# Optimization experiments

Hardware: AMD Instinct MI355X
Metric: run time of the kernel (lower is better)

The kernel has to match this reference:

```python
import jax, jax.numpy as jnp
from jax import lax
import numpy as np

BLOCK = 256
EPS = 1e-6


def rms_norm(x, w):
    var = jnp.mean(jnp.square(x), axis=-1, keepdims=True)
    return x * lax.rsqrt(var + EPS) * w


def lightning_attn(q, k, v, slope):
    # q,k,v: [b,h,n,d]; slope: [h] positive decay rates
    b, h, n, d = q.shape
    nb = n // BLOCK
    ar = jnp.arange(1, BLOCK + 1, dtype=q.dtype)          # [BLOCK]
    s = slope[:, None, None]                               # [h,1,1]
    q_decay = jnp.exp(-s * ar[:, None])                    # [h,BLOCK,1]
    k_decay = jnp.exp(-s * (BLOCK - ar)[:, None])          # [h,BLOCK,1]
    idx = ar[:, None] - ar[None, :]                        # [BLOCK,BLOCK]
    diag_decay = jnp.exp(jnp.where(idx >= 0, -s * idx, -jnp.inf))  # [h,B,B]
    block_decay = jnp.exp(-slope * BLOCK)[None, :, None, None]     # [1,h,1,1]

    def to_blocks(x):
        return jnp.moveaxis(x.reshape(b, h, nb, BLOCK, d), 2, 0)   # [nb,b,h,B,d]

    qb, kb, vb = to_blocks(q), to_blocks(k), to_blocks(v)

    def step(kv, blk):
        qi, ki, vi = blk                                   # [b,h,B,d]
        inter = jnp.einsum('bhmd,bhde->bhme', qi * q_decay, kv)
        qk = jnp.einsum('bhmd,bhkd->bhmk', qi, ki) * diag_decay
        intra = jnp.einsum('bhmk,bhke->bhme', qk, vi)
        kv_new = block_decay * kv + jnp.einsum('bhmd,bhme->bhde', ki * k_decay, vi)
        return kv_new, inter + intra

    kv0 = jnp.zeros((b, h, d, d), q.dtype)
    kv, out = lax.scan(step, kv0, (qb, kb, vb))            # out: [nb,b,h,B,d]
    out = jnp.moveaxis(out, 0, 2).reshape(b, h, n, d)
    return out, kv


def setup_inputs() -> dict:
    key = jax.random.key(0)
    ks = jax.random.split(key, 6)
    b, n, hidden, h, dh = 2, 4096, 2048, 16, 128
    return {
        'hidden_states': jax.random.normal(ks[0], (b, n, hidden), jnp.float32),
        'slope_rate': jax.random.uniform(ks[1], (h,), jnp.float32, 1e-3, 0.2),
        'w_qkv': jax.random.normal(ks[2], (3 * h * dh, hidden), jnp.float32) * 0.02,
        'w_gate': jax.random.normal(ks[3], (h * dh, hidden), jnp.float32) * 0.02,
        'w_out': jax.random.normal(ks[4], (hidden, h * dh), jnp.float32) * 0.02,
        'norm_w': jnp.ones((h * dh,), jnp.float32),
    }


def reference(hidden_states, slope_rate, w_qkv, w_gate, w_out, norm_w):
    b, n, hidden = hidden_states.shape
    h = slope_rate.shape[0]
    dh = hidden // h
    qkv = jax.nn.silu(hidden_states @ w_qkv.T)             # [b,n,3*h*dh]
    qkv = qkv.reshape(b, n, 3, h, dh)
    q = jnp.transpose(qkv[:, :, 0], (0, 2, 1, 3))          # [b,h,n,dh]
    k = jnp.transpose(qkv[:, :, 1], (0, 2, 1, 3))
    v = jnp.transpose(qkv[:, :, 2], (0, 2, 1, 3))
    attn_out, _kv = lightning_attn(q, k, v, slope_rate)
    attn_out = jnp.transpose(attn_out, (0, 2, 1, 3)).reshape(b, n, h * dh)
    out = rms_norm(attn_out, norm_w)
    gate = jax.nn.sigmoid(hidden_states @ w_gate.T)
    out = (gate * out) @ w_out.T
    return out
```

## Files before the change

### kernel.cpp

```cpp
#include <hip/hip_runtime.h>


typedef unsigned short u16;
typedef __bf16 bf16x8 __attribute__((ext_vector_type(8)));
typedef float f32x4 __attribute__((ext_vector_type(4)));

#define SEQ 4096
#define HID 2048

__device__ __forceinline__ u16 f2bf(float f) {
    union { float f; unsigned u; } v; v.f = f;
    unsigned r = v.u + 0x7fffu + ((v.u >> 16) & 1u);
    return (u16)(r >> 16);
}
__device__ __forceinline__ float bf2f(u16 u) {
    union { unsigned u; float f; } v; v.u = ((unsigned)u) << 16; return v.f;
}

typedef __attribute__((address_space(1))) unsigned char gas_u8;
typedef __attribute__((address_space(3))) unsigned char las_u8;
__device__ __forceinline__ void gld16(const void* g, void* l) {
    __builtin_amdgcn_global_load_lds((gas_u8*)g, (las_u8*)l, 16, 0, 0);
}

__global__ __launch_bounds__(256) void castk(const float* __restrict__ in,
                                             u16* __restrict__ out) {
    const size_t i = (size_t)blockIdx.x * 256 + threadIdx.x;
    const float4 f = *(const float4*)&in[i * 4];
    uint2 o;
    o.x = (unsigned)f2bf(f.x) | ((unsigned)f2bf(f.y) << 16);
    o.y = (unsigned)f2bf(f.z) | ((unsigned)f2bf(f.w) << 16);
    *(uint2*)&out[i * 4] = o;
}

template <int MODE>
__global__ __launch_bounds__(512, 2) void gemm256(const u16* __restrict__ A,
                                                  const u16* __restrict__ Bm,
                                                  void* __restrict__ Cv,
                                                  void* __restrict__ aux,
                                                  void* __restrict__ aux2) {
    constexpr int NTN = (MODE == 0) ? 32 : 8;
    constexpr int NWG = (MODE == 0) ? 1024 : 256;
    constexpr int NT  = 32;
    extern __shared__ u16 smem[];

    const int bid  = blockIdx.x;
    const int wgid = (bid & 7) * (NWG >> 3) + (bid >> 3);
    const int tm = wgid / NTN, tn = wgid % NTN;

    const int tid  = threadIdx.x;
    const int lane = tid & 63, wv = tid >> 6;
    const int quad = lane >> 4, cl = lane & 15;
    const int wm = (wv & 1) * 128, wn = (wv >> 1) * 64;

    const int srw  = tid >> 3;
    const int colo = ((tid & 7) ^ (srw & 7)) * 8;
    const u16* gA0 = A  + (size_t)(tm * 256 + srw) * HID + colo;
    const u16* gB0 = Bm + (size_t)(tn * 256 + srw) * HID + colo;

    const int x0 = ((quad       ^ (cl & 7)) * 8);
    const int x1 = (((4 + quad) ^ (cl & 7)) * 8);

    f32x4 acc[8][4];
    const f32x4 zero = {0.f, 0.f, 0.f, 0.f};
    #pragma unroll
    for (int a = 0; a < 8; a++)
        #pragma unroll
        for (int b = 0; b < 4; b++) acc[a][b] = zero;

    bf16x8 af[8], b0[4], b1[4];

    auto STG = [&](int kt, int mat, int hh) {
        const u16* g = (mat ? gB0 : gA0) + (size_t)(hh * 128) * HID + kt * 64;
        u16* l = smem + (kt & 1) * 32768 + mat * 16384 + hh * 8192 + wv * 512;
        gld16(g, l);
        gld16(g + (size_t)64 * HID, l + 4096);
    };
    auto LDA = [&](int qm, int ab) {
        #pragma unroll
        for (int mi = 0; mi < 4; mi++) {
            const int rr = (wm + qm * 64 + mi * 16 + cl) * 64 + ab;
            af[mi * 2 + 0] = *(const bf16x8*)&smem[rr + x0];
            af[mi * 2 + 1] = *(const bf16x8*)&smem[rr + x1];
        }
    };
    auto LDB = [&](bf16x8* d, int qn, int bb2) {
        #pragma unroll
        for (int ni = 0; ni < 2; ni++) {
            const int rr = (wn + qn * 32 + ni * 16 + cl) * 64 + bb2;
            d[ni * 2 + 0] = *(const bf16x8*)&smem[rr + x0];
            d[ni * 2 + 1] = *(const bf16x8*)&smem[rr + x1];
        }
    };
    auto MM = [&](int qm, int qn, const bf16x8* bv) {
        #pragma unroll
        for (int mi = 0; mi < 4; mi++)
            #pragma unroll
            for (int ni = 0; ni < 2; ni++) {
                f32x4 c = acc[qm * 4 + mi][qn * 2 + ni];
                c = __builtin_amdgcn_mfma_f32_16x16x32_bf16(af[mi * 2 + 0], bv[ni * 2 + 0], c, 0, 0, 0);
                c = __builtin_amdgcn_mfma_f32_16x16x32_bf16(af[mi * 2 + 1], bv[ni * 2 + 1], c, 0, 0, 0);
                acc[qm * 4 + mi][qn * 2 + ni] = c;
            }
    };

    STG(0, 1, 0); STG(0, 1, 1); STG(0, 0, 0); STG(0, 0, 1);
    STG(1, 1, 0); STG(1, 1, 1); STG(1, 0, 0);
    asm volatile("s_waitcnt vmcnt(6)" ::: "memory");
    __builtin_amdgcn_s_barrier();

    #pragma unroll 2
    for (int t = 0; t < NT; ++t) {
        const int ab  = (t & 1) * 32768;
        const int bb2 = ab + 16384;
        LDA(0, ab); LDB(b0, 0, bb2);
        if (t + 1 < NT) STG(t + 1, 0, 1);
        __builtin_amdgcn_s_barrier();
        asm volatile("s_waitcnt lgkmcnt(0)" ::: "memory");
        __builtin_amdgcn_s_setprio(1); MM(0, 0, b0); __builtin_amdgcn_s_setprio(0);
        __builtin_amdgcn_s_barrier();
        LDB(b1, 1, bb2);
        if (t + 2 < NT) STG(t + 2, 1, 0);
        __builtin_amdgcn_s_barrier();
        asm volatile("s_waitcnt lgkmcnt(0)" ::: "memory");
        __builtin_amdgcn_s_setprio(1); MM(0, 1, b1); __builtin_amdgcn_s_setprio(0);
        __builtin_amdgcn_s_barrier();
        LDA(1, ab);
        if (t + 2 < NT) STG(t + 2, 1, 1);
        __builtin_amdgcn_s_barrier();
        asm volatile("s_waitcnt lgkmcnt(0)" ::: "memory");
        __builtin_amdgcn_s_setprio(1); MM(1, 1, b1); __builtin_amdgcn_s_setprio(0);
        __builtin_amdgcn_s_barrier();
        if (t + 2 < NT) {
            STG(t + 2, 0, 0);
            asm volatile("s_waitcnt vmcnt(6)" ::: "memory");
        } else {
            asm volatile("s_waitcnt vmcnt(0)" ::: "memory");
        }
        __builtin_amdgcn_s_barrier();
        __builtin_amdgcn_s_setprio(1); MM(1, 0, b0); __builtin_amdgcn_s_setprio(0);
        __builtin_amdgcn_s_barrier();
    }

    if constexpr (MODE == 0) {
        const int grp = tn * 2 + (wn >> 7);
        const int which = grp >> 4, hd = grp & 15;
        const int n64 = wn & 64;
        if (which == 2) {
            const size_t bz = (size_t)((tm >> 4) * 256 + hd * 16 + (tm & 15));
            u16* tdst = (u16*)aux + bz * 32768;
            #pragma unroll
            for (int a = 0; a < 8; a++) {
                const int mm = wm + (a >> 2) * 64 + (a & 3) * 16 + quad * 4;
                #pragma unroll
                for (int b = 0; b < 4; b++) {
                    const int d = n64 + (b >> 1) * 32 + (b & 1) * 16 + cl;
                    u16 p[4];
                    #pragma unroll
                    for (int r = 0; r < 4; r++) {
                        const float x = acc[a][b][r];
                        p[r] = f2bf(x / (1.f + __expf(-x)));
                    }
                    uint2 pk;
                    pk.x = (unsigned)p[0] | ((unsigned)p[1] << 16);
                    pk.y = (unsigned)p[2] | ((unsigned)p[3] << 16);
                    *(uint2*)&tdst[(size_t)d * 256 + mm] = pk;
                }
            }
            return;
        }
        u16* dst = (which == 0) ? (u16*)Cv
                 : (which == 1) ? (u16*)Cv + (size_t)16777216
                                : (u16*)aux2;
        #pragma unroll
        for (int a = 0; a < 8; a++)
            #pragma unroll
            for (int b = 0; b < 4; b++)
                #pragma unroll
                for (int r = 0; r < 4; r++) {
                    const int m = tm * 256 + wm + (a >> 2) * 64 + (a & 3) * 16 + quad * 4 + r;
                    const int col = hd * 128 + n64 + (b >> 1) * 32 + (b & 1) * 16 + cl;
                    const float x = acc[a][b][r];
                    const float v = (which == 3) ? 1.f / (1.f + __expf(-x))
                                                 : x / (1.f + __expf(-x));
                    dst[(size_t)m * HID + col] = f2bf(v);
                }
        return;
    } else {
        float* C = (float*)Cv;
        #pragma unroll
        for (int a = 0; a < 8; a++)
            #pragma unroll
            for (int b = 0; b < 4; b++)
                #pragma unroll
                for (int r = 0; r < 4; r++) {
                    const int m = tm * 256 + wm + (a >> 2) * 64 + (a & 3) * 16 + quad * 4 + r;
                    const int n = tn * 256 + wn + (b >> 1) * 32 + (b & 1) * 16 + cl;
                    C[(size_t)m * HID + n] = acc[a][b][r];
                }
    }
}

#define M_QKV   0
#define M_P     2
#define M_INTRA 3
#define M_KVT   4
#define M_OUT   6

template <int MODE>
__global__ __launch_bounds__(256) void gemm_nt(const u16* __restrict__ A,
                                               const u16* __restrict__ Bm,
                                               void* __restrict__ Cv,
                                               const float* __restrict__ slope,
                                               int bz0,
                                               void* __restrict__ aux,
                                               void* __restrict__ aux2) {
    constexpr int NPH = (MODE == M_INTRA) ? 2 : 1;
    const int tid = threadIdx.x;
    const int tm = blockIdx.x, tn = blockIdx.y;
    const int bzl = blockIdx.z;
    const int bz  = bzl + bz0;

    int bb = 0, hh = 0, jb = 0;
    if constexpr (MODE == M_P || MODE == M_INTRA || MODE == M_KVT) {
        bb = bz >> 8; hh = (bz >> 4) & 15; jb = bz & 15;
    }

    if constexpr (MODE == M_P) {
        if (tn > tm) {
            u16* C = (u16*)Cv + (size_t)bzl * 65536 + tm * 128 * 256 + tn * 128;
            uint4 z = make_uint4(0u, 0u, 0u, 0u);
            #pragma unroll
            for (int i = 0; i < 8; i++) {
                int f = tid + 256 * i;
                int row = f >> 4, c8 = (f & 15) * 8;
                *(uint4*)&C[row * 256 + c8] = z;
            }
            return;
        }
    }

    __shared__ u16 smem[8192];
    u16 (*As)[32] = (u16(*)[32])smem;
    u16 (*Bs)[32] = (u16(*)[32])(smem + 4096);

    const int lane = tid & 63, wv = tid >> 6;
    const int wm = (wv & 1) * 64, wn = (wv >> 1) * 64;
    const int quad = lane >> 4, cl = lane & 15;
    const int lr = lane >> 2;
    const int lc = (lane & 3) * 8;
    u16* lA = &As[wv * 32][0];
    u16* lB = &Bs[wv * 32][0];

    f32x4 acc[4][4];
    const f32x4 zero = {0.f, 0.f, 0.f, 0.f};
    #pragma unroll
    for (int mi = 0; mi < 4; mi++)
        #pragma unroll
        for (int ni = 0; ni < 4; ni++) acc[mi][ni] = zero;

    #pragma unroll
    for (int ph = 0; ph < NPH; ph++) {
        const u16* Ab; const u16* Bb; int lda, ldb, kmax;
        if constexpr (MODE == M_QKV || MODE == M_OUT) {
            Ab = A; lda = HID; Bb = Bm; ldb = HID; kmax = 2048;
        } else if constexpr (MODE == M_P) {
            const size_t o = ((size_t)(bb * SEQ + jb * 256)) * HID + hh * 128;
            Ab = A + o; lda = HID;
            Bb = Bm + o; ldb = HID;
            kmax = 128;
        } else if constexpr (MODE == M_KVT) {
            Ab = A + (size_t)bz * 32768; lda = 256;
            Bb = Bm + (size_t)bz * 32768; ldb = 256;
            kmax = 256;
        } else {
            if (ph == 0) {
                Ab = A + ((size_t)(bb * SEQ + jb * 256)) * HID + hh * 128; lda = HID;
                Bb = Bm + (size_t)bz * 16384; ldb = 128;
                kmax = 128;
            } else {
                Ab = (const u16*)aux + (size_t)bzl * 65536; lda = 256;
                Bb = (const u16*)aux2 + (size_t)bz * 32768; ldb = 256;
                kmax = (tm == 0) ? 128 : 256;
            }
        }
        const u16* gA = Ab + (size_t)(tm * 128 + wv * 32 + lr) * lda + lc;
        const u16* gB = Bb + (size_t)(tn * 128 + wv * 32 + lr) * ldb + lc;

        for (int k0 = 0; k0 < kmax; k0 += 32) {
            __syncthreads();
            gld16(gA + k0,                    lA);
            gld16(gA + k0 + (size_t)16 * lda, lA + 16 * 32);
            gld16(gB + k0,                    lB);
            gld16(gB + k0 + (size_t)16 * ldb, lB + 16 * 32);
            __syncthreads();
            const int ko = quad * 8;
            bf16x8 af[4], bfv[4];
            #pragma unroll
            for (int mi = 0; mi < 4; mi++) af[mi] = *(const bf16x8*)&As[wm + mi * 16 + cl][ko];
            #pragma unroll
            for (int ni = 0; ni < 4; ni++) bfv[ni] = *(const bf16x8*)&Bs[wn + ni * 16 + cl][ko];
            #pragma unroll
            for (int mi = 0; mi < 4; mi++)
                #pragma unroll
                for (int ni = 0; ni < 4; ni++)
                    acc[mi][ni] = __builtin_amdgcn_mfma_f32_16x16x32_bf16(af[mi], bfv[ni], acc[mi][ni], 0, 0, 0);
        }

        if constexpr (MODE == M_INTRA) {
            if (ph == 0) {
                const float s_ = slope[hh];
                #pragma unroll
                for (int mi = 0; mi < 4; mi++)
                    #pragma unroll
                    for (int r = 0; r < 4; r++) {
                        const int m = tm * 128 + wm + mi * 16 + quad * 4 + r;
                        const float qd = __expf(-s_ * (float)(m + 1));
                        #pragma unroll
                        for (int ni = 0; ni < 4; ni++) acc[mi][ni][r] *= qd;
                    }
            }
        }
    }

    float sl = 0.f;
    if constexpr (MODE == M_P) sl = slope[hh];

    #pragma unroll
    for (int mi = 0; mi < 4; mi++) {
        #pragma unroll
        for (int ni = 0; ni < 4; ni++) {
            const f32x4 v = acc[mi][ni];
            #pragma unroll
            for (int r = 0; r < 4; r++) {
                const int m = tm * 128 + wm + mi * 16 + quad * 4 + r;
                const int n = tn * 128 + wn + ni * 16 + cl;
                const float x = v[r];
                if constexpr (MODE == M_P) {
                    const int d = m - n;
                    ((u16*)Cv)[(size_t)bzl * 65536 + m * 256 + n] =
                        f2bf(d >= 0 ? x * __expf(-sl * (float)d) : 0.f);
                } else if constexpr (MODE == M_INTRA) {
                    ((u16*)Cv)[((size_t)(bb * SEQ + jb * 256 + m)) * HID + hh * 128 + n] = f2bf(x);
                } else if constexpr (MODE == M_KVT) {
                    ((float*)Cv)[(size_t)bz * 16384 + m * 128 + n] = x;
                } else {
                    ((float*)Cv)[(size_t)m * HID + n] = x;
                }
            }
        }
    }
}

__global__ __launch_bounds__(256) void transpose_k(const u16* __restrict__ kb,
                                                   u16* __restrict__ kTs,
                                                   const float* __restrict__ slope) {
    __shared__ u16 t[128][137];
    const int bz = blockIdx.x;
    const int bb = bz >> 8, hh = (bz >> 4) & 15, jb = bz & 15;
    const int tid = threadIdx.x;
    const float s_ = slope[hh];
    const u16* src = kb + ((size_t)(bb * SEQ + jb * 256)) * HID + hh * 128;
    u16* dst = kTs + (size_t)bz * 32768;

    for (int half = 0; half < 2; half++) {
        #pragma unroll
        for (int i = 0; i < 8; i++) {
            const int flat = tid + 256 * i;
            const int row = flat >> 4, c8 = (flat & 15) * 8;
            *(uint4*)&t[row][c8] = *(const uint4*)&src[(size_t)(half * 128 + row) * HID + c8];
        }
        __syncthreads();
        #pragma unroll
        for (int i = 0; i < 8; i++) {
            const int flat = tid + 256 * i;
            const int d = flat >> 4, mc = (flat & 15) * 8;
            u16 p[8];
            #pragma unroll
            for (int j = 0; j < 8; j++) {
                const int m = half * 128 + mc + j;
                p[j] = f2bf(bf2f(t[mc + j][d]) * __expf(-s_ * (float)(255 - m)));
            }
            uint4 pk;
            pk.x = (unsigned)p[0] | ((unsigned)p[1] << 16);
            pk.y = (unsigned)p[2] | ((unsigned)p[3] << 16);
            pk.z = (unsigned)p[4] | ((unsigned)p[5] << 16);
            pk.w = (unsigned)p[6] | ((unsigned)p[7] << 16);
            *(uint4*)&dst[(size_t)d * 256 + half * 128 + mc] = pk;
        }
        __syncthreads();
    }
}

__global__ __launch_bounds__(256) void scan_kv(const float* __restrict__ KVT,
                                               u16* __restrict__ ST,
                                               const float* __restrict__ slope) {
    const int bh = blockIdx.x >> 4, ch = blockIdx.x & 15;
    const int off = ch * 1024 + threadIdx.x * 4;
    const float bd = __expf(-256.f * slope[bh & 15]);
    float4 st = {0.f, 0.f, 0.f, 0.f};
    for (int j = 0; j < 16; j++) {
        const size_t base = ((size_t)(bh * 16 + j)) * 16384 + off;
        uint2 o;
        o.x = (unsigned)f2bf(st.x) | ((unsigned)f2bf(st.y) << 16);
        o.y = (unsigned)f2bf(st.z) | ((unsigned)f2bf(st.w) << 16);
        *(uint2*)&ST[base] = o;
        const float4 kv = *(const float4*)&KVT[base];
        st.x = bd * st.x + kv.x;
        st.y = bd * st.y + kv.y;
        st.z = bd * st.z + kv.z;
        st.w = bd * st.w + kv.w;
    }
}

__global__ __launch_bounds__(256) void rmsnorm_gate(const u16* __restrict__ attn,
                                                    const u16* __restrict__ gate,
                                                    const float* __restrict__ nw,
                                                    u16* __restrict__ y) {
    const int r = blockIdx.x, tid = threadIdx.x;
    const size_t base = (size_t)r * HID + tid * 8;
    const uint4 a = *(const uint4*)&attn[base];
    float x[8];
    x[0] = bf2f(a.x & 0xffff); x[1] = bf2f(a.x >> 16);
    x[2] = bf2f(a.y & 0xffff); x[3] = bf2f(a.y >> 16);
    x[4] = bf2f(a.z & 0xffff); x[5] = bf2f(a.z >> 16);
    x[6] = bf2f(a.w & 0xffff); x[7] = bf2f(a.w >> 16);
    float s = 0.f;
    #pragma unroll
    for (int i = 0; i < 8; i++) s += x[i] * x[i];
    #pragma unroll
    for (int off = 32; off > 0; off >>= 1) s += __shfl_down(s, off);
    __shared__ float red[4];
    if ((tid & 63) == 0) red[tid >> 6] = s;
    __syncthreads();
    const float tot = red[0] + red[1] + red[2] + red[3];
    const float sc = rsqrtf(tot * (1.f / 2048.f) + 1e-6f);
    const uint4 g = *(const uint4*)&gate[base];
    float gv[8];
    gv[0] = bf2f(g.x & 0xffff); gv[1] = bf2f(g.x >> 16);
    gv[2] = bf2f(g.y & 0xffff); gv[3] = bf2f(g.y >> 16);
    gv[4] = bf2f(g.z & 0xffff); gv[5] = bf2f(g.z >> 16);
    gv[6] = bf2f(g.w & 0xffff); gv[7] = bf2f(g.w >> 16);
    const float4 w0 = *(const float4*)&nw[tid * 8];
    const float4 w1 = *(const float4*)&nw[tid * 8 + 4];
    const float wv[8] = {w0.x, w0.y, w0.z, w0.w, w1.x, w1.y, w1.z, w1.w};
    u16 o[8];
    #pragma unroll
    for (int i = 0; i < 8; i++) o[i] = f2bf(gv[i] * x[i] * sc * wv[i]);
    uint4 ov;
    ov.x = (unsigned)o[0] | ((unsigned)o[1] << 16);
    ov.y = (unsigned)o[2] | ((unsigned)o[3] << 16);
    ov.z = (unsigned)o[4] | ((unsigned)o[5] << 16);
    ov.w = (unsigned)o[6] | ((unsigned)o[7] << 16);
    *(uint4*)&y[base] = ov;
}

extern "C" void kernel_launch(void* const* d_in, const int* in_sizes, int n_in,
                              void* d_out, int out_size, void* d_ws, size_t ws_size,
                              hipStream_t stream) {
    const float* hidden = (const float*)d_in[0];
    const float* slope  = (const float*)d_in[1];
    const float* w_qkv  = (const float*)d_in[2];
    const float* w_gate = (const float*)d_in[3];
    const float* w_out  = (const float*)d_in[4];
    const float* norm_w = (const float*)d_in[5];
    float* out = (float*)d_out;

    char* w = (char*)d_ws;
    u16* qb   = (u16*)(w);
    u16* kb   = (u16*)(w +  33554432);
    u16* kTs  = (u16*)(w +  67108864);
    u16* hid_bf = (u16*)(w + 100663296);
    u16* vT   = (u16*)(w + 134217728);
    u16* gate = (u16*)(w + 167772160);
    u16* wqkv_bf  = (u16*)(w + 201326592);
    u16* wgate_bf = (u16*)(w + 201326592 + 25165824);
    float* KVT  = (float*)hid_bf;
    u16*   ST   = kTs;
    u16*   P    = hid_bf;
    u16*   wout_bf = kb;
    u16*   attn = wqkv_bf;
    u16*   y    = kTs;

    static bool s_attr = false;
    if (!s_attr) {
        (void)hipFuncSetAttribute((const void*)gemm256<0>,
                                  hipFuncAttributeMaxDynamicSharedMemorySize, 131072);
        (void)hipFuncSetAttribute((const void*)gemm256<1>,
                                  hipFuncAttributeMaxDynamicSharedMemorySize, 131072);
        s_attr = true;
    }

    castk<<<16384, 256, 0, stream>>>(hidden, hid_bf);
    castk<<<12288, 256, 0, stream>>>(w_qkv,  wqkv_bf);
    castk<<< 4096, 256, 0, stream>>>(w_gate, wgate_bf);

    gemm256<0><<<dim3(1024), dim3(512), 131072, stream>>>(hid_bf, wqkv_bf, qb, vT, gate);
    transpose_k     <<<512,             256, 0, stream>>>(kb, kTs, slope);
    gemm_nt<M_KVT ><<<dim3(1, 1, 512),  256, 0, stream>>>(vT, kTs, KVT, slope, 0, nullptr, nullptr);
    scan_kv         <<<512,             256, 0, stream>>>(KVT, ST, slope);
    gemm_nt<M_P   ><<<dim3(2, 2, 256),  256, 0, stream>>>(qb, kb, P, slope, 0, nullptr, nullptr);
    gemm_nt<M_INTRA><<<dim3(2, 1, 256), 256, 0, stream>>>(qb, ST, attn, slope, 0, P, vT);
    gemm_nt<M_P   ><<<dim3(2, 2, 256),  256, 0, stream>>>(qb, kb, P, slope, 256, nullptr, nullptr);
    gemm_nt<M_INTRA><<<dim3(2, 1, 256), 256, 0, stream>>>(qb, ST, attn, slope, 256, P, vT);
    castk<<< 4096, 256, 0, stream>>>(w_out, wout_bf);
    rmsnorm_gate    <<<8192,            256, 0, stream>>>(attn, gate, norm_w, y);
    gemm256<1><<<dim3(256), dim3(512), 131072, stream>>>(y, wout_bf, (void*)out, nullptr, nullptr);
}
```

Baseline: 495.6 us.

## Restructure gemm256 main loop into ping-pong fragment pipeline and remap tiles per XCD

The 256x256 GEMM main loop is rewritten so LDS fragment reads for the next quadrant and next k-tile are issued while the current MFMA block runs. It uses two A-fragment register sets that alternate between iterations, with fewer barriers and waits per tile. It also changes the block-to-tile mapping in MODE 0 so each XCD works on a compact group of M rows, which should improve L2 reuse. The added register pressure and the vmcnt(0) wait in every tile could cost occupancy or stall on global loads.

```diff
diff --git a/kernel.cpp b/kernel.cpp
--- a/kernel.cpp
+++ b/kernel.cpp
@@ -40,13 +40,19 @@
                                                   void* __restrict__ aux,
                                                   void* __restrict__ aux2) {
     constexpr int NTN = (MODE == 0) ? 32 : 8;
-    constexpr int NWG = (MODE == 0) ? 1024 : 256;
     constexpr int NT  = 32;
     extern __shared__ u16 smem[];
 
-    const int bid  = blockIdx.x;
-    const int wgid = (bid & 7) * (NWG >> 3) + (bid >> 3);
-    const int tm = wgid / NTN, tn = wgid % NTN;
+    const int bid = blockIdx.x;
+    const int xcd = bid & 7, l = bid >> 3;
+    int tm, tn;
+    if constexpr (MODE == 0) {
+        tm = xcd * 4 + (l & 3);
+        tn = ((l >> 2) & 7) | ((l >> 5) << 3);
+    } else {
+        const int wgid = xcd * 32 + l;
+        tm = wgid / NTN; tn = wgid % NTN;
+    }
 
     const int tid  = threadIdx.x;
     const int lane = tid & 63, wv = tid >> 6;
@@ -68,78 +74,93 @@
         #pragma unroll
         for (int b = 0; b < 4; b++) acc[a][b] = zero;
 
-    bf16x8 af[8], b0[4], b1[4];
+    bf16x8 afA[8], afB[8], b0[4], b1[4];
 
     auto STG = [&](int kt, int mat, int hh) {
         const u16* g = (mat ? gB0 : gA0) + (size_t)(hh * 128) * HID + kt * 64;
-        u16* l = smem + (kt & 1) * 32768 + mat * 16384 + hh * 8192 + wv * 512;
-        gld16(g, l);
-        gld16(g + (size_t)64 * HID, l + 4096);
+        u16* lp = smem + (kt & 1) * 32768 + mat * 16384 + hh * 8192 + wv * 512;
+        gld16(g, lp);
+        gld16(g + (size_t)64 * HID, lp + 4096);
     };
-    auto LDA = [&](int qm, int ab) {
-        #pragma unroll
-        for (int mi = 0; mi < 4; mi++) {
-            const int rr = (wm + qm * 64 + mi * 16 + cl) * 64 + ab;
-            af[mi * 2 + 0] = *(const bf16x8*)&smem[rr + x0];
-            af[mi * 2 + 1] = *(const bf16x8*)&smem[rr + x1];
-        }
-    };
-    auto LDB = [&](bf16x8* d, int qn, int bb2) {
-        #pragma unroll
-        for (int ni = 0; ni < 2; ni++) {
-            const int rr = (wn + qn * 32 + ni * 16 + cl) * 64 + bb2;
-            d[ni * 2 + 0] = *(const bf16x8*)&smem[rr + x0];
-            d[ni * 2 + 1] = *(const bf16x8*)&smem[rr + x1];
-        }
-    };
-    auto MM = [&](int qm, int qn, const bf16x8* bv) {
-        #pragma unroll
-        for (int mi = 0; mi < 4; mi++)
-            #pragma unroll
-            for (int ni = 0; ni < 2; ni++) {
-                f32x4 c = acc[qm * 4 + mi][qn * 2 + ni];
-                c = __builtin_amdgcn_mfma_f32_16x16x32_bf16(af[mi * 2 + 0], bv[ni * 2 + 0], c, 0, 0, 0);
-                c = __builtin_amdgcn_mfma_f32_16x16x32_bf16(af[mi * 2 + 1], bv[ni * 2 + 1], c, 0, 0, 0);
-                acc[qm * 4 + mi][qn * 2 + ni] = c;
-            }
-    };
+
+#define LDA_(D, qm, ab)                                                      \
+    {                                                                        \
+        _Pragma("unroll")                                                    \
+        for (int mi = 0; mi < 4; mi++) {                                     \
+            const int rr = (wm + (qm) * 64 + mi * 16 + cl) * 64 + (ab);      \
+            D[mi * 2 + 0] = *(const bf16x8*)&smem[rr + x0];                  \
+            D[mi * 2 + 1] = *(const bf16x8*)&smem[rr + x1];                  \
+        }                                                                    \
+    }
+#define LDB_(D, qn, bb)                                                      \
+    {                                                                        \
+        _Pragma("unroll")                                                    \
+        for (int ni = 0; ni < 2; ni++) {                                     \
+            const int rr = (wn + (qn) * 32 + ni * 16 + cl) * 64 + (bb);      \
+            D[ni * 2 + 0] = *(const bf16x8*)&smem[rr + x0];                  \
+            D[ni * 2 + 1] = *(const bf16x8*)&smem[rr + x1];                  \
+        }                                                                    \
+    }
+#define MM_(Af, Bf, qm, qn)                                                  \
+    {                                                                        \
+        _Pragma("unroll")                                                    \
+        for (int mi = 0; mi < 4; mi++)                                       \
+            _Pragma("unroll")                                                \
+            for (int ni = 0; ni < 2; ni++) {                                 \
+                f32x4 c = acc[(qm) * 4 + mi][(qn) * 2 + ni];                 \
+                c = __builtin_amdgcn_mfma_f32_16x16x32_bf16(Af[mi * 2 + 0], Bf[ni * 2 + 0], c, 0, 0, 0); \
+                c = __builtin_amdgcn_mfma_f32_16x16x32_bf16(Af[mi * 2 + 1], Bf[ni * 2 + 1], c, 0, 0, 0); \
+                acc[(qm) * 4 + mi][(qn) * 2 + ni] = c;                       \
+            }                                                                \
+    }
+
+#define TILE_(t, AF0, AF1)                                                   \
+    {                                                                        \
+        const int ab  = ((t) & 1) * 32768;                                   \
+        const int bb2 = ab + 16384;                                          \
+        const int nab = (((t) + 1) & 1) * 32768;                             \
+                                                                    \
+        LDA_(AF1, 1, ab);                                                    \
+        LDB_(b1, 1, bb2);                                                    \
+        asm volatile("s_waitcnt lgkmcnt(12)" ::: "memory");                  \
+        __builtin_amdgcn_sched_barrier(0);                                   \
+        __builtin_amdgcn_s_barrier();                                        \
+        __builtin_amdgcn_s_setprio(1);                                       \
+        MM_(AF0, b0, 0, 0);                                                  \
+        __builtin_amdgcn_s_setprio(0);                                       \
+                                                                    \
+        asm volatile("s_waitcnt vmcnt(0) lgkmcnt(0)" ::: "memory");          \
+        __builtin_amdgcn_sched_barrier(0);                                   \
+        __builtin_amdgcn_s_barrier();                                        \
+        __builtin_amdgcn_s_setprio(1);                                       \
+        MM_(AF1, b0, 1, 0);                                                  \
+        __builtin_amdgcn_s_setprio(0);                                       \
+                                                                    \
+        if ((t) + 2 < NT) { STG((t) + 2, 1, 0); STG((t) + 2, 1, 1); }        \
+        if ((t) + 1 < NT) LDB_(b0, 0, nab + 16384);                          \
+        __builtin_amdgcn_s_barrier();                                        \
+        __builtin_amdgcn_s_setprio(1);                                       \
+        MM_(AF1, b1, 1, 1);                                                  \
+        __builtin_amdgcn_s_setprio(0);                                       \
+                                                                    \
+        if ((t) + 2 < NT) { STG((t) + 2, 0, 0); STG((t) + 2, 0, 1); }        \
+        if ((t) + 1 < NT) LDA_(AF1, 0, nab);                                 \
+        __builtin_amdgcn_s_barrier();                                        \
+        __builtin_amdgcn_s_setprio(1);                                       \
+        MM_(AF0, b1, 0, 1);                                                  \
+        __builtin_amdgcn_s_setprio(0);                                       \
+    }
 
     STG(0, 1, 0); STG(0, 1, 1); STG(0, 0, 0); STG(0, 0, 1);
-    STG(1, 1, 0); STG(1, 1, 1); STG(1, 0, 0);
-    asm volatile("s_waitcnt vmcnt(6)" ::: "memory");
+    STG(1, 1, 0); STG(1, 1, 1); STG(1, 0, 0); STG(1, 0, 1);
+    asm volatile("s_waitcnt vmcnt(8)" ::: "memory");
     __builtin_amdgcn_s_barrier();
-
-    #pragma unroll 2
-    for (int t = 0; t < NT; ++t) {
-        const int ab  = (t & 1) * 32768;
-        const int bb2 = ab + 16384;
-        LDA(0, ab); LDB(b0, 0, bb2);
-        if (t + 1 < NT) STG(t + 1, 0, 1);
-        __builtin_amdgcn_s_barrier();
-        asm volatile("s_waitcnt lgkmcnt(0)" ::: "memory");
-        __builtin_amdgcn_s_setprio(1); MM(0, 0, b0); __builtin_amdgcn_s_setprio(0);
-        __builtin_amdgcn_s_barrier();
-        LDB(b1, 1, bb2);
-        if (t + 2 < NT) STG(t + 2, 1, 0);
-        __builtin_amdgcn_s_barrier();
-        asm volatile("s_waitcnt lgkmcnt(0)" ::: "memory");
-        __builtin_amdgcn_s_setprio(1); MM(0, 1, b1); __builtin_amdgcn_s_setprio(0);
-        __builtin_amdgcn_s_barrier();
-        LDA(1, ab);
-        if (t + 2 < NT) STG(t + 2, 1, 1);
-        __builtin_amdgcn_s_barrier();
-        asm volatile("s_waitcnt lgkmcnt(0)" ::: "memory");
-        __builtin_amdgcn_s_setprio(1); MM(1, 1, b1); __builtin_amdgcn_s_setprio(0);
-        __builtin_amdgcn_s_barrier();
-        if (t + 2 < NT) {
-            STG(t + 2, 0, 0);
-            asm volatile("s_waitcnt vmcnt(6)" ::: "memory");
-        } else {
-            asm volatile("s_waitcnt vmcnt(0)" ::: "memory");
-        }
-        __builtin_amdgcn_s_barrier();
-        __builtin_amdgcn_s_setprio(1); MM(1, 0, b0); __builtin_amdgcn_s_setprio(0);
-        __builtin_amdgcn_s_barrier();
+    LDB_(b0, 0, 16384);
+    LDA_(afA, 0, 0);
+
+    for (int t = 0; t < NT; t += 2) {
+        TILE_(t,     afA, afB);
+        TILE_(t + 1, afB, afA);
     }
 
     if constexpr (MODE == 0) {
@@ -199,6 +220,10 @@
                     C[(size_t)m * HID + n] = acc[a][b][r];
                 }
     }
+#undef TILE_
+#undef MM_
+#undef LDB_
+#undef LDA_
 }
 
 #define M_QKV   0
```

New measurement: 625.5 us. +26.2%, slower.
